# Kernel tuning notes

Measured on AMD Instinct MI355X. Metric: run time of the kernel, lower is better.

## Reference

```python
import jax, jax.numpy as jnp
import numpy as np

N = 8192
IN_F = 512
OUT_F = 64
NEG_SLOPE = 0.01  # nn.LeakyReLU default
MASK_VAL = -1e9


def setup_inputs() -> dict:
    key = jax.random.key(0)
    k_h, k_adj, k_W, k_a = jax.random.split(key, 4)
    h = jax.random.normal(k_h, (N, IN_F), dtype=jnp.float32)
    adjacency = jax.random.randint(k_adj, (N, N), 0, 2, dtype=jnp.int32)
    # xavier_uniform bounds
    bW = float(np.sqrt(6.0 / (IN_F + OUT_F)))
    ba = float(np.sqrt(6.0 / (2 * OUT_F + 1)))
    W = jax.random.uniform(k_W, (IN_F, OUT_F), minval=-bW, maxval=bW, dtype=jnp.float32)
    a = jax.random.uniform(k_a, (2 * OUT_F, 1), minval=-ba, maxval=ba, dtype=jnp.float32)
    return {"h": h, "adjacency": adjacency, "W": W, "a": a}


def reference(h, adjacency, W, a):
    WH = h @ W                                  # [N, out_f]
    wh1 = WH @ a[:OUT_F, :]                     # [N, 1]
    wh2 = WH @ a[OUT_F:, :]                     # [N, 1]
    e = jax.nn.leaky_relu(wh1 + wh2.T, negative_slope=NEG_SLOPE)  # [N, N]
    attnt = jnp.where(adjacency > 0, e, jnp.float32(MASK_VAL))
    attnt = jax.nn.softmax(attnt, axis=1)       # row-wise softmax
    hfirst = attnt @ WH                         # [N, out_f]
    return jax.nn.elu(hfirst)
```

## Files before the change

### kernel.cpp

```cpp
#include <hip/hip_runtime.h>
#include <hip/hip_bf16.h>

#define N 8192
#define IN_F 512
#define OUT_F 64
#define S_SPLIT 16
#define JT (N / S_SPLIT)
#define LDP 536
#define LOG2E 1.44269504088896340736f

typedef __attribute__((ext_vector_type(8))) short short8;
typedef __attribute__((ext_vector_type(4))) float floatx4;
typedef __attribute__((ext_vector_type(4))) int intx4;

__device__ inline short f2bf(float x) {
    __hip_bfloat16 b = __float2bfloat16(x);
    return __builtin_bit_cast(short, b);
}

__device__ inline float fexp2(float x) {
#if __has_builtin(__builtin_amdgcn_exp2f)
    return __builtin_amdgcn_exp2f(x);
#else
    return exp2f(x);
#endif
}

__global__ void k_wt(const float* __restrict__ W, short* __restrict__ WT) {
    int idx = blockIdx.x * 256 + threadIdx.x;
    int k = idx >> 6, f = idx & 63;
    WT[f * IN_F + k] = f2bf(W[k * OUT_F + f]);
}

__global__ __launch_bounds__(64) void k_wh(const float* __restrict__ h,
                                           const short* __restrict__ WT,
                                           const float* __restrict__ a,
                                           short* __restrict__ WHbT,
                                           float* __restrict__ wh1,
                                           float* __restrict__ wh2) {
    __shared__ float tile[OUT_F][17];
    int lane = threadIdx.x;
    int n = lane & 15, q = lane >> 4;
    int i0 = blockIdx.x * 16;
    int rowA = i0 + n;
    const float* hp = h + (size_t)rowA * IN_F + q * 8;
    floatx4 acc[4] = {};
#pragma unroll
    for (int k0 = 0; k0 < IN_F; k0 += 32) {
        floatx4 h0 = *(const floatx4*)(hp + k0);
        floatx4 h1 = *(const floatx4*)(hp + k0 + 4);
        short8 af;
#pragma unroll
        for (int j = 0; j < 4; j++) { af[j] = f2bf(h0[j]); af[j + 4] = f2bf(h1[j]); }
#pragma unroll
        for (int b = 0; b < 4; b++) {
            short8 bf_ = *(const short8*)(WT + (b * 16 + n) * IN_F + k0 + q * 8);
            acc[b] = __builtin_amdgcn_mfma_f32_16x16x32_bf16(af, bf_, acc[b], 0, 0, 0);
        }
    }
#pragma unroll
    for (int b = 0; b < 4; b++)
#pragma unroll
        for (int r = 0; r < 4; r++)
            tile[b * 16 + n][q * 4 + r] = acc[b][r];
    float a1v[4], a2v[4];
#pragma unroll
    for (int b = 0; b < 4; b++) { a1v[b] = a[b * 16 + n]; a2v[b] = a[OUT_F + b * 16 + n]; }
#pragma unroll
    for (int r = 0; r < 4; r++) {
        float s1 = 0.f, s2 = 0.f;
#pragma unroll
        for (int b = 0; b < 4; b++) { s1 += acc[b][r] * a1v[b]; s2 += acc[b][r] * a2v[b]; }
#pragma unroll
        for (int m = 1; m <= 8; m <<= 1) {
            s1 += __shfl_xor(s1, m, 64);
            s2 += __shfl_xor(s2, m, 64);
        }
        if (n == 0) {
            wh1[i0 + q * 4 + r] = s1 * LOG2E;
            wh2[i0 + q * 4 + r] = s2 * LOG2E;
        }
    }
    __syncthreads();
    const float* tc = tile[lane];
    short8 s0, s1v;
#pragma unroll
    for (int k = 0; k < 8; k++) { s0[k] = f2bf(tc[k]); s1v[k] = f2bf(tc[k + 8]); }
    *(short8*)(WHbT + (size_t)lane * N + i0) = s0;
    *(short8*)(WHbT + (size_t)lane * N + i0 + 8) = s1v;
}

__global__ __launch_bounds__(256, 2) void k_attn(const int* __restrict__ adj,
                                                 const short* __restrict__ WHbT,
                                                 const float* __restrict__ wh1,
                                                 const float* __restrict__ wh2,
                                                 float* __restrict__ num_part,
                                                 float* __restrict__ den_part) {
    __shared__ short ldsb[OUT_F * LDP];
    int tid = threadIdx.x;
    int w = tid >> 6;
    int lane = tid & 63;
    int n = lane & 15, q = lane >> 4;
    int split = blockIdx.y;
    int j0 = split * JT;
    int i0 = blockIdx.x * 256 + w * 64;

#pragma unroll
    for (int l = 0; l < 16; l++) {
        int idx = l * 256 + tid;
        int f = idx >> 6, c16 = idx & 63;
        short8 v = *(const short8*)(WHbT + (size_t)f * N + j0 + c16 * 8);
        *(short8*)(ldsb + f * LDP + c16 * 8) = v;
    }
    __syncthreads();

    float wh1f[4];
#pragma unroll
    for (int rf = 0; rf < 4; rf++) wh1f[rf] = wh1[i0 + rf * 16 + n];

    floatx4 acc[4][4] = {};
    floatx4 accd[4] = {};
    const float* w2p = wh2 + j0 + q * 8;
    const short* lp = ldsb + q * 8;

    short8 onesf = {};
    if (n == 0) {
        short o = f2bf(1.0f);
#pragma unroll
        for (int jj = 0; jj < 8; jj++) onesf[jj] = o;
    }

    const int* ap = adj + j0 + q * 8;
    size_t roff[4];
#pragma unroll
    for (int rf = 0; rf < 4; rf++) roff[rf] = (size_t)(i0 + rf * 16 + n) * N;

    intx4 A0[4], A1[4], B0[4], B1[4];

    auto loads = [&](intx4* D0, intx4* D1, int s) {
#pragma unroll
        for (int rf = 0; rf < 4; rf++) {
            const int* pp = ap + roff[rf] + s * 32;
            D0[rf] = *(const intx4*)pp;
            D1[rf] = *(const intx4*)(pp + 4);
        }
    };

    auto step = [&](const intx4* D0, const intx4* D1, int s) {
        floatx4 w20 = *(const floatx4*)(w2p + s * 32);
        floatx4 w21 = *(const floatx4*)(w2p + s * 32 + 4);
        short8 bfr[4];
#pragma unroll
        for (int b = 0; b < 4; b++)
            bfr[b] = *(const short8*)(lp + (b * 16 + n) * LDP + s * 32);
#pragma unroll
        for (int rf = 0; rf < 4; rf++) {
            float p[8];
#pragma unroll
            for (int jj = 0; jj < 8; jj++) {
                float e = wh1f[rf] + ((jj < 4) ? w20[jj] : w21[jj - 4]);
                float el = fmaxf(e, 0.01f * e);
                int av = (jj < 4) ? D0[rf][jj] : D1[rf][jj - 4];
                el = (av > 0) ? el : -1024.0f;
                p[jj] = fexp2(el);
            }
            short8 af;
#pragma unroll
            for (int jj = 0; jj < 8; jj++) af[jj] = f2bf(p[jj]);
#pragma unroll
            for (int b = 0; b < 4; b++)
                acc[rf][b] = __builtin_amdgcn_mfma_f32_16x16x32_bf16(af, bfr[b], acc[rf][b], 0, 0, 0);
            accd[rf] = __builtin_amdgcn_mfma_f32_16x16x32_bf16(af, onesf, accd[rf], 0, 0, 0);
        }
    };

    loads(A0, A1, 0);
    for (int sp = 0; sp < 8; sp++) {
        int s0 = sp * 2;
        loads(B0, B1, s0 + 1);
        step(A0, A1, s0);
        loads(A0, A1, (s0 + 2) & 15);
        step(B0, B1, s0 + 1);
    }

#pragma unroll
    for (int rf = 0; rf < 4; rf++)
        if (n == 0)
            *(floatx4*)(den_part + (size_t)split * N + i0 + rf * 16 + q * 4) = accd[rf];

    float* np_ = num_part + (size_t)split * N * OUT_F;
#pragma unroll
    for (int rf = 0; rf < 4; rf++)
#pragma unroll
        for (int b = 0; b < 4; b++)
#pragma unroll
            for (int r = 0; r < 4; r++)
                np_[(size_t)(i0 + rf * 16 + q * 4 + r) * OUT_F + b * 16 + n] = acc[rf][b][r];
}

__global__ void k_final(const float* __restrict__ num_part,
                        const float* __restrict__ den_part,
                        float* __restrict__ out) {
    int idx = blockIdx.x * 256 + threadIdx.x;
    int row = idx >> 6;
    float s = 0.f, d = 0.f;
#pragma unroll
    for (int sp = 0; sp < S_SPLIT; sp++) {
        s += num_part[(size_t)sp * N * OUT_F + idx];
        d += den_part[sp * N + row];
    }
    float x = s / d;
    out[idx] = (x > 0.f) ? x : (__expf(x) - 1.f);
}

extern "C" void kernel_launch(void* const* d_in, const int* in_sizes, int n_in,
                              void* d_out, int out_size, void* d_ws, size_t ws_size,
                              hipStream_t stream) {
    const float* h = (const float*)d_in[0];
    const int* adj = (const int*)d_in[1];
    const float* W = (const float*)d_in[2];
    const float* a = (const float*)d_in[3];
    float* out = (float*)d_out;

    char* ws = (char*)d_ws;
    short* WHbT     = (short*)(ws);
    short* WT       = (short*)(ws + (size_t)(1 << 20));
    float* wh1      = (float*)(ws + (size_t)(1 << 20) + (64 << 10));
    float* wh2      = wh1 + N;
    float* num_p    = (float*)(ws + (size_t)(16 << 20));
    float* den_p    = (float*)(ws + (size_t)(48 << 20));

    k_wt<<<dim3(128), dim3(256), 0, stream>>>(W, WT);
    k_wh<<<dim3(N / 16), dim3(64), 0, stream>>>(h, WT, a, WHbT, wh1, wh2);
    k_attn<<<dim3(N / 256, S_SPLIT), dim3(256), 0, stream>>>(adj, WHbT, wh1, wh2,
                                                             num_p, den_p);
    k_final<<<dim3((N * OUT_F) / 256), dim3(256), 0, stream>>>(num_p, den_p, out);
}
```

Before: 406.2 us.

## Shrink row tile per wave and iterate column sub-chunks with fewer splits

Each wave now handles 16 rows instead of 64, so a block covers 64 rows, and the column split drops from 16 to 4. Each block loops over 512-wide column sub-chunks, reloading the WH tile into LDS for each one. The intent is to cut the partial-sum traffic written and read in the final reduction, and to lower register pressure so more blocks fit per CU. In exchange, each WH tile in LDS is reused by fewer rows, so WHbT is reloaded more often and extra barriers are added per sub-chunk.

New measurement: 441.3 us. +8.7%, slower.

```diff
diff --git a/kernel.cpp b/kernel.cpp
--- a/kernel.cpp
+++ b/kernel.cpp
@@ -4,8 +4,10 @@
 #define N 8192
 #define IN_F 512
 #define OUT_F 64
-#define S_SPLIT 16
+#define S_SPLIT 4
 #define JT (N / S_SPLIT)
+#define SUBC 512
+#define NSUB (JT / SUBC)
 #define LDP 536
 #define LOG2E 1.44269504088896340736f
 
@@ -103,24 +105,12 @@
     int n = lane & 15, q = lane >> 4;
     int split = blockIdx.y;
     int j0 = split * JT;
-    int i0 = blockIdx.x * 256 + w * 64;
-
-#pragma unroll
-    for (int l = 0; l < 16; l++) {
-        int idx = l * 256 + tid;
-        int f = idx >> 6, c16 = idx & 63;
-        short8 v = *(const short8*)(WHbT + (size_t)f * N + j0 + c16 * 8);
-        *(short8*)(ldsb + f * LDP + c16 * 8) = v;
-    }
-    __syncthreads();
-
-    float wh1f[4];
-#pragma unroll
-    for (int rf = 0; rf < 4; rf++) wh1f[rf] = wh1[i0 + rf * 16 + n];
-
-    floatx4 acc[4][4] = {};
-    floatx4 accd[4] = {};
-    const float* w2p = wh2 + j0 + q * 8;
+    int i0 = blockIdx.x * 64 + w * 16;
+
+    float wh1f = wh1[i0 + n];
+
+    floatx4 acc[4] = {};
+    floatx4 accd = {};
     const short* lp = ldsb + q * 8;
 
     short8 onesf = {};
@@ -130,72 +120,77 @@
         for (int jj = 0; jj < 8; jj++) onesf[jj] = o;
     }
 
-    const int* ap = adj + j0 + q * 8;
-    size_t roff[4];
-#pragma unroll
-    for (int rf = 0; rf < 4; rf++) roff[rf] = (size_t)(i0 + rf * 16 + n) * N;
-
-    intx4 A0[4], A1[4], B0[4], B1[4];
-
-    auto loads = [&](intx4* D0, intx4* D1, int s) {
-#pragma unroll
-        for (int rf = 0; rf < 4; rf++) {
-            const int* pp = ap + roff[rf] + s * 32;
-            D0[rf] = *(const intx4*)pp;
-            D1[rf] = *(const intx4*)(pp + 4);
-        }
+    const int* rowp = adj + (size_t)(i0 + n) * N + j0 + q * 8;
+
+    intx4 A0, A1, B0, B1;
+
+    auto loads = [&](intx4& D0, intx4& D1, int sub, int s) {
+        const int* pp = rowp + sub * SUBC + s * 32;
+        D0 = *(const intx4*)pp;
+        D1 = *(const intx4*)(pp + 4);
     };
 
-    auto step = [&](const intx4* D0, const intx4* D1, int s) {
+    auto step = [&](const intx4& D0, const intx4& D1, const float* w2p, int s) {
         floatx4 w20 = *(const floatx4*)(w2p + s * 32);
         floatx4 w21 = *(const floatx4*)(w2p + s * 32 + 4);
         short8 bfr[4];
 #pragma unroll
         for (int b = 0; b < 4; b++)
             bfr[b] = *(const short8*)(lp + (b * 16 + n) * LDP + s * 32);
-#pragma unroll
-        for (int rf = 0; rf < 4; rf++) {
-            float p[8];
-#pragma unroll
-            for (int jj = 0; jj < 8; jj++) {
-                float e = wh1f[rf] + ((jj < 4) ? w20[jj] : w21[jj - 4]);
-                float el = fmaxf(e, 0.01f * e);
-                int av = (jj < 4) ? D0[rf][jj] : D1[rf][jj - 4];
-                el = (av > 0) ? el : -1024.0f;
-                p[jj] = fexp2(el);
+        float p[8];
+#pragma unroll
+        for (int jj = 0; jj < 8; jj++) {
+            float e = wh1f + ((jj < 4) ? w20[jj] : w21[jj - 4]);
+            float el = fmaxf(e, 0.01f * e);
+            int av = (jj < 4) ? D0[jj] : D1[jj - 4];
+            el = (av > 0) ? el : -1024.0f;
+            p[jj] = fexp2(el);
+        }
+        short8 af;
+#pragma unroll
+        for (int jj = 0; jj < 8; jj++) af[jj] = f2bf(p[jj]);
+#pragma unroll
+        for (int b = 0; b < 4; b++)
+            acc[b] = __builtin_amdgcn_mfma_f32_16x16x32_bf16(af, bfr[b], acc[b], 0, 0, 0);
+        accd = __builtin_amdgcn_mfma_f32_16x16x32_bf16(af, onesf, accd, 0, 0, 0);
+    };
+
+    loads(A0, A1, 0, 0);
+    for (int sub = 0; sub < NSUB; sub++) {
+        __syncthreads();
+#pragma unroll
+        for (int l = 0; l < 16; l++) {
+            int idx = l * 256 + tid;
+            int f = idx >> 6, c16 = idx & 63;
+            short8 v = *(const short8*)(WHbT + (size_t)f * N + j0 + sub * SUBC + c16 * 8);
+            *(short8*)(ldsb + f * LDP + c16 * 8) = v;
+        }
+        __syncthreads();
+
+        const float* w2p = wh2 + j0 + sub * SUBC + q * 8;
+#pragma unroll
+        for (int sp = 0; sp < 8; sp++) {
+            int s0 = sp * 2;
+            loads(B0, B1, sub, s0 + 1);
+            step(A0, A1, w2p, s0);
+            if (sp < 7) {
+                loads(A0, A1, sub, s0 + 2);
+            } else {
+                loads(A0, A1, (sub + 1) & (NSUB - 1), 0);
             }
-            short8 af;
-#pragma unroll
-            for (int jj = 0; jj < 8; jj++) af[jj] = f2bf(p[jj]);
-#pragma unroll
-            for (int b = 0; b < 4; b++)
-                acc[rf][b] = __builtin_amdgcn_mfma_f32_16x16x32_bf16(af, bfr[b], acc[rf][b], 0, 0, 0);
-            accd[rf] = __builtin_amdgcn_mfma_f32_16x16x32_bf16(af, onesf, accd[rf], 0, 0, 0);
-        }
-    };
-
-    loads(A0, A1, 0);
-    for (int sp = 0; sp < 8; sp++) {
-        int s0 = sp * 2;
-        loads(B0, B1, s0 + 1);
-        step(A0, A1, s0);
-        loads(A0, A1, (s0 + 2) & 15);
-        step(B0, B1, s0 + 1);
-    }
-
-#pragma unroll
-    for (int rf = 0; rf < 4; rf++)
-        if (n == 0)
-            *(floatx4*)(den_part + (size_t)split * N + i0 + rf * 16 + q * 4) = accd[rf];
+            step(B0, B1, w2p, s0 + 1);
+        }
+    }
+
+    if (n == 0)
+        *(floatx4*)(den_part + (size_t)split * N + i0 + q * 4) = accd;
 
     float* np_ = num_part + (size_t)split * N * OUT_F;
 #pragma unroll
-    for (int rf = 0; rf < 4; rf++)
-#pragma unroll
-        for (int b = 0; b < 4; b++)
-#pragma unroll
-            for (int r = 0; r < 4; r++)
-                np_[(size_t)(i0 + rf * 16 + q * 4 + r) * OUT_F + b * 16 + n] = acc[rf][b][r];
+    for (int b = 0; b < 4; b++)
+#pragma unroll
+        for (int r = 0; r < 4; r++)
+            np_[(size_t)(i0 + q * 4 + r) * OUT_F + b * 16 + n] = acc[b][r];
 }
 
 __global__ void k_final(const float* __restrict__ num_part,
@@ -232,7 +227,7 @@
 
     k_wt<<<dim3(128), dim3(256), 0, stream>>>(W, WT);
     k_wh<<<dim3(N / 16), dim3(64), 0, stream>>>(h, WT, a, WHbT, wh1, wh2);
-    k_attn<<<dim3(N / 256, S_SPLIT), dim3(256), 0, stream>>>(adj, WHbT, wh1, wh2,
-                                                             num_p, den_p);
+    k_attn<<<dim3(N / 64, S_SPLIT), dim3(256), 0, stream>>>(adj, WHbT, wh1, wh2,
+                                                            num_p, den_p);
     k_final<<<dim3((N * OUT_F) / 256), dim3(256), 0, stream>>>(num_p, den_p, out);
 }
```
